# Kernel tuning notes

Hardware: AMD Instinct MI355X
Metric: run time of the kernel (lower is better)

The kernel has to match this reference:

```python
import jax, jax.numpy as jnp
import numpy as np

HIDDEN = 4096
NUM_HEADS = 32
HEAD_DIM = HIDDEN // NUM_HEADS  # 128


def apply_rope(x, cos, sin):
    # x: (B, H, S, D); cos/sin: (S, D//2)
    d2 = x.shape[-1] // 2
    x1, x2 = x[..., :d2], x[..., d2:]
    c = cos[None, None, :x.shape[2], :]
    s = sin[None, None, :x.shape[2], :]
    return jnp.concatenate([x1 * c - x2 * s, x2 * c + x1 * s], axis=-1)


def setup_inputs() -> dict:
    key = jax.random.key(0)
    ks = jax.random.split(key, 7)
    B, S = 2, 2048
    scale = 1.0 / np.sqrt(HIDDEN)
    return {
        "x": jax.random.normal(ks[0], (B, S, HIDDEN), dtype=jnp.float32),
        "cos": jax.random.normal(ks[1], (S, HEAD_DIM // 2), dtype=jnp.float32),
        "sin": jax.random.normal(ks[2], (S, HEAD_DIM // 2), dtype=jnp.float32),
        "wq": jax.random.normal(ks[3], (HIDDEN, HIDDEN), dtype=jnp.float32) * scale,
        "wk": jax.random.normal(ks[4], (HIDDEN, HIDDEN), dtype=jnp.float32) * scale,
        "wv": jax.random.normal(ks[5], (HIDDEN, HIDDEN), dtype=jnp.float32) * scale,
        "wo": jax.random.normal(ks[6], (HIDDEN, HIDDEN), dtype=jnp.float32) * scale,
    }


def reference(x, cos, sin, wq, wk, wv, wo):
    B, S, _ = x.shape
    # nn.Linear(x) = x @ W.T  (weights stored (out, in))
    def proj(w):
        t = jnp.einsum('bsd,ed->bse', x, w)
        return t.reshape(B, S, NUM_HEADS, HEAD_DIM).transpose(0, 2, 1, 3)
    q, k, v = proj(wq), proj(wk), proj(wv)
    q = apply_rope(q, cos, sin)
    k = apply_rope(k, cos, sin)
    scale = HEAD_DIM ** (-0.5)
    attn = jnp.einsum('bhqd,bhkd->bhqk', q, k) * scale  # (B,H,S,S)
    causal = jnp.tril(jnp.ones((S, S), dtype=bool))
    attn = jnp.where(causal[None, None], attn, -jnp.inf)
    attn = jax.nn.softmax(attn, axis=-1)
    out = jnp.einsum('bhqk,bhkd->bhqd', attn, v)
    out = out.transpose(0, 2, 1, 3).reshape(B, S, HIDDEN)
    return jnp.einsum('bsd,ed->bse', out, wo)
```

## Files before the change

### kernel.cpp

```cpp
#include <hip/hip_runtime.h>
#include <stdint.h>

#define DEV __device__ __forceinline__

typedef __attribute__((ext_vector_type(8))) short short8v;
typedef __attribute__((ext_vector_type(4))) short short4v;
typedef __attribute__((ext_vector_type(4))) float f32x4;
typedef __attribute__((ext_vector_type(16))) float f32x16;

DEV uint16_t f2bf(float f) {
  union { float f; uint32_t u; } x; x.f = f;
  return (uint16_t)((x.u + 0x7FFFu + ((x.u >> 16) & 1u)) >> 16);
}
DEV float bf2f(uint16_t v) {
  union { uint32_t u; float f; } x; x.u = ((uint32_t)v) << 16;
  return x.f;
}

DEV void gload_lds16(const uint16_t* g, uint16_t* l) {
  __builtin_amdgcn_global_load_lds(
      (const __attribute__((address_space(1))) uint32_t*)g,
      (__attribute__((address_space(3))) uint32_t*)l, 16, 0, 0);
}

__global__ void convert5_kernel(const float* __restrict__ x,
                                const float* __restrict__ wq,
                                const float* __restrict__ wk,
                                const float* __restrict__ wv,
                                const float* __restrict__ wo,
                                uint16_t* __restrict__ xb, uint16_t* __restrict__ wqb,
                                uint16_t* __restrict__ wkb, uint16_t* __restrict__ wvb,
                                uint16_t* __restrict__ wob, int n4) {
  const int which = blockIdx.y;
  const float* in = which == 0 ? x : which == 1 ? wq : which == 2 ? wk
                                   : which == 3 ? wv : wo;
  uint16_t* out = which == 0 ? xb : which == 1 ? wqb : which == 2 ? wkb
                                  : which == 3 ? wvb : wob;
  int i = blockIdx.x * blockDim.x + threadIdx.x;
  if (i >= n4) return;
  float4 v = reinterpret_cast<const float4*>(in)[i];
  short4v o;
  o[0] = (short)f2bf(v.x); o[1] = (short)f2bf(v.y);
  o[2] = (short)f2bf(v.z); o[3] = (short)f2bf(v.w);
  *reinterpret_cast<short4v*>(out + (size_t)i * 4) = o;
}

template <int F32OUT>
__global__ __launch_bounds__(512, 2) void gemm256_kernel(
    const uint16_t* __restrict__ A, const uint16_t* __restrict__ Bt,
    float* __restrict__ Cf, uint16_t* __restrict__ Cb, int M, int N, int K) {
  __shared__ uint16_t smem[65536];
  uint16_t* As0 = smem;
  uint16_t* As1 = smem + 16384;
  uint16_t* Bs0 = smem + 32768;
  uint16_t* Bs1 = smem + 49152;

  const int tid = threadIdx.x;
  const int lane = tid & 63, w = tid >> 6;
  const int ln16 = lane & 15, g = lane >> 4;
  const int wr = w >> 2, wc = w & 3;

  const int nbx = gridDim.x;
  int bid = blockIdx.y * nbx + blockIdx.x;
  int nb = nbx * gridDim.y;
  int cpx = nb >> 3;
  int sw = (bid & 7) * cpx + (bid >> 3);
  const int m0 = (sw / nbx) * 256, n0 = (sw % nbx) * 256;

  const int trow = tid >> 3;
  const int tcol = ((tid & 7) ^ (trow & 7)) * 8;
  const uint16_t* srcA = A + (size_t)(m0 + trow) * K + tcol;
  const int brow = (w >> 2) * 64 + (w & 3) * 8 + (lane >> 3);
  const int bcol = ((lane & 7) ^ ((lane >> 3) & 7)) * 8;
  const uint16_t* srcB = Bt + (size_t)(n0 + brow) * K + bcol;
  const int dstAw = w * 512;
  const int dstBw = ((w >> 2) * 64 + (w & 3) * 8) * 64;

#define STA(buf, q, kt) \
  gload_lds16(srcA + (size_t)((q) * 64) * K + (kt) * 64, (buf) + (q) * 4096 + dstAw)
#define STB(buf, nq, c, kt) \
  gload_lds16(srcB + (size_t)((c) * 128 + (nq) * 32) * K + (kt) * 64, \
              (buf) + ((c) * 128 + (nq) * 32) * 64 + dstBw)
#define LDA(buf, mq, mi, ks) \
  (*reinterpret_cast<const short8v*>( \
      (buf) + (wr * 128 + (mq) * 64 + (mi) * 16 + ln16) * 64 + \
      ((((ks) * 4 + g) ^ (ln16 & 7)) * 8)))
#define LDB(buf, nq, ni, ks) \
  (*reinterpret_cast<const short8v*>( \
      (buf) + (wc * 64 + (nq) * 32 + (ni) * 16 + ln16) * 64 + \
      ((((ks) * 4 + g) ^ (ln16 & 7)) * 8)))

  f32x4 acc[8][4];
#pragma unroll
  for (int i = 0; i < 8; ++i)
#pragma unroll
    for (int j = 0; j < 4; ++j) acc[i][j] = f32x4{0.f, 0.f, 0.f, 0.f};

  STA(As0, 0, 0); STA(As0, 2, 0); STA(As0, 1, 0); STA(As0, 3, 0);
  STB(Bs0, 0, 0, 0); STB(Bs0, 0, 1, 0); STB(Bs0, 1, 0, 0); STB(Bs0, 1, 1, 0);
  STA(As1, 0, 1); STA(As1, 2, 1);
  STB(Bs1, 0, 0, 1); STB(Bs1, 0, 1, 1); STB(Bs1, 1, 0, 1); STB(Bs1, 1, 1, 1);
  asm volatile("s_waitcnt vmcnt(6)" ::: "memory");
  __builtin_amdgcn_sched_barrier(0);
  __builtin_amdgcn_s_barrier();

  uint16_t *Ac = As0, *An = As1, *Bc = Bs0, *Bn = Bs1;
  short8v af[4][2], bf0[2][2], bf1[2][2];

  const int NT = K >> 6;
  for (int t = 0; t < NT; ++t) {
    const int k1 = (t + 1 < NT) ? t + 1 : NT - 1;
    const int k2 = (t + 2 < NT) ? t + 2 : NT - 1;
#pragma unroll
    for (int mi = 0; mi < 4; ++mi) { af[mi][0] = LDA(Ac, 0, mi, 0); af[mi][1] = LDA(Ac, 0, mi, 1); }
#pragma unroll
    for (int ni = 0; ni < 2; ++ni) { bf0[ni][0] = LDB(Bc, 0, ni, 0); bf0[ni][1] = LDB(Bc, 0, ni, 1); }
    STA(An, 1, k1); STA(An, 3, k1);
    __builtin_amdgcn_s_barrier();
    asm volatile("s_waitcnt lgkmcnt(0)" ::: "memory");
    __builtin_amdgcn_sched_barrier(0);
    __builtin_amdgcn_s_setprio(1);
#pragma unroll
    for (int ks = 0; ks < 2; ++ks)
#pragma unroll
      for (int mi = 0; mi < 4; ++mi)
#pragma unroll
        for (int ni = 0; ni < 2; ++ni)
          acc[mi][ni] = __builtin_amdgcn_mfma_f32_16x16x32_bf16(af[mi][ks], bf0[ni][ks], acc[mi][ni], 0, 0, 0);
    __builtin_amdgcn_s_setprio(0);
    __builtin_amdgcn_s_barrier();
#pragma unroll
    for (int ni = 0; ni < 2; ++ni) { bf1[ni][0] = LDB(Bc, 1, ni, 0); bf1[ni][1] = LDB(Bc, 1, ni, 1); }
    STA(Ac, 0, k2); STA(Ac, 2, k2);
    __builtin_amdgcn_s_barrier();
    asm volatile("s_waitcnt lgkmcnt(0)" ::: "memory");
    __builtin_amdgcn_sched_barrier(0);
    __builtin_amdgcn_s_setprio(1);
#pragma unroll
    for (int ks = 0; ks < 2; ++ks)
#pragma unroll
      for (int mi = 0; mi < 4; ++mi)
#pragma unroll
        for (int ni = 0; ni < 2; ++ni)
          acc[mi][2 + ni] = __builtin_amdgcn_mfma_f32_16x16x32_bf16(af[mi][ks], bf1[ni][ks], acc[mi][2 + ni], 0, 0, 0);
    __builtin_amdgcn_s_setprio(0);
    __builtin_amdgcn_s_barrier();
#pragma unroll
    for (int mi = 0; mi < 4; ++mi) { af[mi][0] = LDA(Ac, 1, mi, 0); af[mi][1] = LDA(Ac, 1, mi, 1); }
    STB(Bc, 0, 0, k2); STB(Bc, 0, 1, k2);
    __builtin_amdgcn_s_barrier();
    asm volatile("s_waitcnt lgkmcnt(0)" ::: "memory");
    __builtin_amdgcn_sched_barrier(0);
    __builtin_amdgcn_s_setprio(1);
#pragma unroll
    for (int ks = 0; ks < 2; ++ks)
#pragma unroll
      for (int mi = 0; mi < 4; ++mi)
#pragma unroll
        for (int ni = 0; ni < 2; ++ni)
          acc[4 + mi][2 + ni] = __builtin_amdgcn_mfma_f32_16x16x32_bf16(af[mi][ks], bf1[ni][ks], acc[4 + mi][2 + ni], 0, 0, 0);
    __builtin_amdgcn_s_setprio(0);
    __builtin_amdgcn_s_barrier();
    STB(Bc, 1, 0, k2); STB(Bc, 1, 1, k2);
    __builtin_amdgcn_s_barrier();
    __builtin_amdgcn_s_setprio(1);
#pragma unroll
    for (int ks = 0; ks < 2; ++ks)
#pragma unroll
      for (int mi = 0; mi < 4; ++mi)
#pragma unroll
        for (int ni = 0; ni < 2; ++ni)
          acc[4 + mi][ni] = __builtin_amdgcn_mfma_f32_16x16x32_bf16(af[mi][ks], bf0[ni][ks], acc[4 + mi][ni], 0, 0, 0);
    __builtin_amdgcn_s_setprio(0);
    asm volatile("s_waitcnt vmcnt(6)" ::: "memory");
    __builtin_amdgcn_sched_barrier(0);
    __builtin_amdgcn_s_barrier();
    uint16_t* tp = Ac; Ac = An; An = tp;
    tp = Bc; Bc = Bn; Bn = tp;
  }

#pragma unroll
  for (int gmi = 0; gmi < 8; ++gmi)
#pragma unroll
    for (int r = 0; r < 4; ++r) {
      int row = m0 + wr * 128 + gmi * 16 + g * 4 + r;
#pragma unroll
      for (int gni = 0; gni < 4; ++gni) {
        int col = n0 + wc * 64 + gni * 16 + ln16;
        if (F32OUT)
          Cf[(size_t)row * N + col] = acc[gmi][gni][r];
        else
          Cb[(size_t)row * N + col] = (uint16_t)f2bf(acc[gmi][gni][r]);
      }
    }
#undef STA
#undef STB
#undef LDA
#undef LDB
}

__global__ void rope_kernel(uint16_t* __restrict__ buf,
                            const float* __restrict__ cost,
                            const float* __restrict__ sint) {
  int idx = blockIdx.x * blockDim.x + threadIdx.x;
  int j8 = idx & 7;
  int h = (idx >> 3) & 31;
  int s = (idx >> 8) & 2047;
  int b = idx >> 19;
  size_t base = ((size_t)(b * 2048 + s)) * 4096 + h * 128 + j8 * 8;
  short8v x1 = *reinterpret_cast<const short8v*>(buf + base);
  short8v x2 = *reinterpret_cast<const short8v*>(buf + base + 64);
  float4 c0 = *reinterpret_cast<const float4*>(cost + s * 64 + j8 * 8);
  float4 c1 = *reinterpret_cast<const float4*>(cost + s * 64 + j8 * 8 + 4);
  float4 s0 = *reinterpret_cast<const float4*>(sint + s * 64 + j8 * 8);
  float4 s1 = *reinterpret_cast<const float4*>(sint + s * 64 + j8 * 8 + 4);
  float c[8] = {c0.x, c0.y, c0.z, c0.w, c1.x, c1.y, c1.z, c1.w};
  float sn[8] = {s0.x, s0.y, s0.z, s0.w, s1.x, s1.y, s1.z, s1.w};
  short8v o1, o2;
#pragma unroll
  for (int e = 0; e < 8; ++e) {
    float a = bf2f((uint16_t)x1[e]);
    float bb = bf2f((uint16_t)x2[e]);
    o1[e] = (short)f2bf(a * c[e] - bb * sn[e]);
    o2[e] = (short)f2bf(bb * c[e] + a * sn[e]);
  }
  *reinterpret_cast<short8v*>(buf + base) = o1;
  *reinterpret_cast<short8v*>(buf + base + 64) = o2;
}

__global__ __launch_bounds__(256, 2) void flash_kernel(
    const uint16_t* __restrict__ Q, const uint16_t* __restrict__ K,
    const uint16_t* __restrict__ V, uint16_t* __restrict__ O) {
  constexpr int S = 2048, HID = 4096;
  __shared__ uint16_t Ks[64 * 128];
  __shared__ uint16_t Vt[128 * 64];

  const int tid = threadIdx.x;
  const int lane = tid & 63, w = tid >> 6;
  const int l31 = lane & 31, hi = lane >> 5;
  const int bh = blockIdx.y;
  const int b = bh >> 5, h = bh & 31;
  const int bt = 15 - blockIdx.x;
  const int q0 = bt * 128;
  const int q0w = q0 + w * 32;
  const size_t base = (size_t)b * S * HID + (size_t)h * 128;
  const int swz = (l31 & 7) << 3;

  short8v qf[8];
  {
    const uint16_t* qrow = Q + base + (size_t)(q0w + l31) * HID + hi * 8;
#pragma unroll
    for (int c = 0; c < 8; ++c)
      qf[c] = *reinterpret_cast<const short8v*>(qrow + c * 16);
  }

  f32x16 o[4];
#pragma unroll
  for (int db = 0; db < 4; ++db)
#pragma unroll
    for (int r = 0; r < 16; ++r) o[db][r] = 0.f;
  float m_run = -1e30f, l_run = 0.f;
  const float cl2e = 0.12751025f;

  const int ntiles = bt * 2 + 2;
  for (int kt = 0; kt < ntiles; ++kt) {
    const int kb = kt * 64;
    if (kt > 0) __syncthreads();
#pragma unroll
    for (int i = 0; i < 4; ++i) {
      int row = i * 16 + (tid >> 4);
      int colc = (tid & 15) * 8;
      short8v kv = *reinterpret_cast<const short8v*>(
          K + base + (size_t)(kb + row) * HID + colc);
      *reinterpret_cast<short8v*>(Ks + row * 128 + (colc ^ ((row & 7) << 3))) = kv;
    }
    {
      int k4 = tid & 15, dc = tid >> 4;
      short8v v0 = *reinterpret_cast<const short8v*>(V + base + (size_t)(kb + 4 * k4 + 0) * HID + dc * 8);
      short8v v1 = *reinterpret_cast<const short8v*>(V + base + (size_t)(kb + 4 * k4 + 1) * HID + dc * 8);
      short8v v2 = *reinterpret_cast<const short8v*>(V + base + (size_t)(kb + 4 * k4 + 2) * HID + dc * 8);
      short8v v3 = *reinterpret_cast<const short8v*>(V + base + (size_t)(kb + 4 * k4 + 3) * HID + dc * 8);
#pragma unroll
      for (int e = 0; e < 8; ++e) {
        int row = dc * 8 + e;
        short4v pk; pk[0] = v0[e]; pk[1] = v1[e]; pk[2] = v2[e]; pk[3] = v3[e];
        *reinterpret_cast<short4v*>(Vt + row * 64 + ((k4 * 4) ^ ((row & 7) << 3))) = pk;
      }
    }
    __syncthreads();

    if (kb <= q0w + 31) {
      f32x16 s0, s1;
#pragma unroll
      for (int r = 0; r < 16; ++r) { s0[r] = 0.f; s1[r] = 0.f; }
#pragma unroll
      for (int c = 0; c < 8; ++c) {
        int col = c * 16 + hi * 8;
        short8v kf0 = *reinterpret_cast<const short8v*>(Ks + l31 * 128 + (col ^ swz));
        short8v kf1 = *reinterpret_cast<const short8v*>(Ks + (32 + l31) * 128 + (col ^ swz));
        s0 = __builtin_amdgcn_mfma_f32_32x32x16_bf16(kf0, qf[c], s0, 0, 0, 0);
        s1 = __builtin_amdgcn_mfma_f32_32x32x16_bf16(kf1, qf[c], s1, 0, 0, 0);
      }
#pragma unroll
      for (int r = 0; r < 16; ++r) { s0[r] *= cl2e; s1[r] *= cl2e; }
      if (kb + 63 > q0w) {
        const int qg = q0w + l31;
#pragma unroll
        for (int r = 0; r < 16; ++r) {
          int kl = (r & 3) + 8 * (r >> 2) + 4 * hi;
          if (kb + kl > qg) s0[r] = -1e30f;
          if (kb + 32 + kl > qg) s1[r] = -1e30f;
        }
      }
      float mx = s0[0];
#pragma unroll
      for (int r = 1; r < 16; ++r) mx = fmaxf(mx, s0[r]);
#pragma unroll
      for (int r = 0; r < 16; ++r) mx = fmaxf(mx, s1[r]);
      mx = fmaxf(mx, __shfl_xor(mx, 32));
      if (__any(mx > m_run + 8.0f)) {
        float nm = fmaxf(m_run, mx);
        float f = __builtin_amdgcn_exp2f(m_run - nm);
        l_run *= f;
#pragma unroll
        for (int db = 0; db < 4; ++db)
#pragma unroll
          for (int r = 0; r < 16; ++r) o[db][r] *= f;
        m_run = nm;
      }
      float rs = 0.f;
#pragma unroll
      for (int r = 0; r < 16; ++r) { s0[r] = __builtin_amdgcn_exp2f(s0[r] - m_run); rs += s0[r]; }
#pragma unroll
      for (int r = 0; r < 16; ++r) { s1[r] = __builtin_amdgcn_exp2f(s1[r] - m_run); rs += s1[r]; }
      rs += __shfl_xor(rs, 32);
      l_run += rs;
      uint32_t c0[8], c1[8];
#pragma unroll
      for (int i = 0; i < 4; ++i) {
        asm("v_cvt_pk_bf16_f32 %0, %1, %2" : "=v"(c0[i])     : "v"(s0[4 * i]),     "v"(s0[4 * i + 1]));
        asm("v_cvt_pk_bf16_f32 %0, %1, %2" : "=v"(c1[i])     : "v"(s0[4 * i + 2]), "v"(s0[4 * i + 3]));
        asm("v_cvt_pk_bf16_f32 %0, %1, %2" : "=v"(c0[4 + i]) : "v"(s1[4 * i]),     "v"(s1[4 * i + 1]));
        asm("v_cvt_pk_bf16_f32 %0, %1, %2" : "=v"(c1[4 + i]) : "v"(s1[4 * i + 2]), "v"(s1[4 * i + 3]));
      }
      short8v pa[4];
#pragma unroll
      for (int t = 0; t < 4; ++t) {
        int st = t >> 1, ts = t & 1;
        uint32_t a0 = c0[st * 4 + 2 * ts],     a1 = c1[st * 4 + 2 * ts];
        uint32_t b0 = c0[st * 4 + 2 * ts + 1], b1 = c1[st * 4 + 2 * ts + 1];
        uint32_t sb0 = (uint32_t)__shfl_xor((int)b0, 32);
        uint32_t sb1 = (uint32_t)__shfl_xor((int)b1, 32);
        uint32_t sa0 = (uint32_t)__shfl_xor((int)a0, 32);
        uint32_t sa1 = (uint32_t)__shfl_xor((int)a1, 32);
        union { uint32_t u[4]; short8v v; } pk;
        pk.u[0] = hi ? sb0 : a0;
        pk.u[1] = hi ? sb1 : a1;
        pk.u[2] = hi ? b0 : sa0;
        pk.u[3] = hi ? b1 : sa1;
        pa[t] = pk.v;
      }
#pragma unroll
      for (int t = 0; t < 4; ++t) {
        int col = t * 16 + hi * 8;
#pragma unroll
        for (int db = 0; db < 4; ++db) {
          short8v vf = *reinterpret_cast<const short8v*>(
              Vt + (db * 32 + l31) * 64 + (col ^ swz));
          o[db] = __builtin_amdgcn_mfma_f32_32x32x16_bf16(vf, pa[t], o[db], 0, 0, 0);
        }
      }
    }
  }

  float inv = 1.f / l_run;
  uint16_t* orow = O + base + (size_t)(q0w + l31) * HID;
#pragma unroll
  for (int db = 0; db < 4; ++db)
#pragma unroll
    for (int rq = 0; rq < 4; ++rq) {
      short4v st4;
#pragma unroll
      for (int e = 0; e < 4; ++e) st4[e] = (short)f2bf(o[db][rq * 4 + e] * inv);
      *reinterpret_cast<short4v*>(orow + db * 32 + rq * 8 + hi * 4) = st4;
    }
}

extern "C" void kernel_launch(void* const* d_in, const int* in_sizes, int n_in,
                              void* d_out, int out_size, void* d_ws, size_t ws_size,
                              hipStream_t stream) {
  const float* x    = (const float*)d_in[0];
  const float* cosb = (const float*)d_in[1];
  const float* sinb = (const float*)d_in[2];
  const float* wq   = (const float*)d_in[3];
  const float* wk   = (const float*)d_in[4];
  const float* wv   = (const float*)d_in[5];
  const float* wo   = (const float*)d_in[6];
  float* out = (float*)d_out;

  const size_t BUF = 33554432;
  if (ws_size < 8 * BUF) return;
  char* ws = (char*)d_ws;
  uint16_t* xb  = (uint16_t*)(ws + 0 * BUF);
  uint16_t* wqb = (uint16_t*)(ws + 1 * BUF);
  uint16_t* wkb = (uint16_t*)(ws + 2 * BUF);
  uint16_t* wvb = (uint16_t*)(ws + 3 * BUF);
  uint16_t* wob = (uint16_t*)(ws + 4 * BUF);
  uint16_t* qb  = (uint16_t*)(ws + 5 * BUF);
  uint16_t* kb  = (uint16_t*)(ws + 6 * BUF);
  uint16_t* vb  = (uint16_t*)(ws + 7 * BUF);
  uint16_t* ab  = xb;

  const int nElem = 2 * 2048 * 4096;
  dim3 cgrid(nElem / 4 / 256, 5);
  convert5_kernel<<<cgrid, 256, 0, stream>>>(x, wq, wk, wv, wo,
                                             xb, wqb, wkb, wvb, wob, nElem / 4);

  dim3 ggrid(16, 16), gblk(512);
  gemm256_kernel<0><<<ggrid, gblk, 0, stream>>>(xb, wqb, nullptr, qb, 4096, 4096, 4096);
  gemm256_kernel<0><<<ggrid, gblk, 0, stream>>>(xb, wkb, nullptr, kb, 4096, 4096, 4096);
  gemm256_kernel<0><<<ggrid, gblk, 0, stream>>>(xb, wvb, nullptr, vb, 4096, 4096, 4096);

  dim3 rgrid(1048576 / 256);
  rope_kernel<<<rgrid, 256, 0, stream>>>(qb, cosb, sinb);
  rope_kernel<<<rgrid, 256, 0, stream>>>(kb, cosb, sinb);

  dim3 fgrid(16, 64);
  flash_kernel<<<fgrid, 256, 0, stream>>>(qb, kb, vb, ab);

  gemm256_kernel<1><<<ggrid, gblk, 0, stream>>>(ab, wob, out, nullptr, 4096, 4096, 4096);
}
```

Baseline: 786.9 us.

## Prefetch next K/V tile into registers during compute and raise MFMA priority

The flash attention loop now issues global loads for the next K/V tile into registers before computing on the current tile, then writes them to LDS after a barrier. This hides global memory latency behind the QK and PV MFMA work instead of stalling at the start of each iteration. It also wraps the MFMA blocks in s_setprio to favour matrix issue across waves. The cost is higher register pressure from the prefetch buffers, which could hurt occupancy under launch_bounds(256,2).

```diff
diff --git a/kernel.cpp b/kernel.cpp
--- a/kernel.cpp
+++ b/kernel.cpp
@@ -246,6 +246,11 @@
   const size_t base = (size_t)b * S * HID + (size_t)h * 128;
   const int swz = (l31 & 7) << 3;
 
+  const int ksr = tid >> 4;
+  const int ksc = (tid & 15) * 8;
+  const int vk4 = tid & 15;
+  const int vdc = tid >> 4;
+
   short8v qf[8];
   {
     const uint16_t* qrow = Q + base + (size_t)(q0w + l31) * HID + hi * 8;
@@ -262,37 +267,50 @@
   float m_run = -1e30f, l_run = 0.f;
   const float cl2e = 0.12751025f;
 
+  short8v kp[4], vp[4];
+
+#pragma unroll
+  for (int i = 0; i < 4; ++i)
+    kp[i] = *reinterpret_cast<const short8v*>(
+        K + base + (size_t)(i * 16 + ksr) * HID + ksc);
+#pragma unroll
+  for (int j = 0; j < 4; ++j)
+    vp[j] = *reinterpret_cast<const short8v*>(
+        V + base + (size_t)(4 * vk4 + j) * HID + vdc * 8);
+#pragma unroll
+  for (int i = 0; i < 4; ++i) {
+    int row = i * 16 + ksr;
+    *reinterpret_cast<short8v*>(Ks + row * 128 + (ksc ^ ((row & 7) << 3))) = kp[i];
+  }
+#pragma unroll
+  for (int e = 0; e < 8; ++e) {
+    int row = vdc * 8 + e;
+    short4v pk; pk[0] = vp[0][e]; pk[1] = vp[1][e]; pk[2] = vp[2][e]; pk[3] = vp[3][e];
+    *reinterpret_cast<short4v*>(Vt + row * 64 + ((vk4 * 4) ^ ((row & 7) << 3))) = pk;
+  }
+  __syncthreads();
+
   const int ntiles = bt * 2 + 2;
   for (int kt = 0; kt < ntiles; ++kt) {
     const int kb = kt * 64;
-    if (kt > 0) __syncthreads();
-#pragma unroll
-    for (int i = 0; i < 4; ++i) {
-      int row = i * 16 + (tid >> 4);
-      int colc = (tid & 15) * 8;
-      short8v kv = *reinterpret_cast<const short8v*>(
-          K + base + (size_t)(kb + row) * HID + colc);
-      *reinterpret_cast<short8v*>(Ks + row * 128 + (colc ^ ((row & 7) << 3))) = kv;
+    const bool havenext = (kt + 1 < ntiles);
+    if (havenext) {
+      const int kb2 = kb + 64;
+#pragma unroll
+      for (int i = 0; i < 4; ++i)
+        kp[i] = *reinterpret_cast<const short8v*>(
+            K + base + (size_t)(kb2 + i * 16 + ksr) * HID + ksc);
+#pragma unroll
+      for (int j = 0; j < 4; ++j)
+        vp[j] = *reinterpret_cast<const short8v*>(
+            V + base + (size_t)(kb2 + 4 * vk4 + j) * HID + vdc * 8);
     }
-    {
-      int k4 = tid & 15, dc = tid >> 4;
-      short8v v0 = *reinterpret_cast<const short8v*>(V + base + (size_t)(kb + 4 * k4 + 0) * HID + dc * 8);
-      short8v v1 = *reinterpret_cast<const short8v*>(V + base + (size_t)(kb + 4 * k4 + 1) * HID + dc * 8);
-      short8v v2 = *reinterpret_cast<const short8v*>(V + base + (size_t)(kb + 4 * k4 + 2) * HID + dc * 8);
-      short8v v3 = *reinterpret_cast<const short8v*>(V + base + (size_t)(kb + 4 * k4 + 3) * HID + dc * 8);
-#pragma unroll
-      for (int e = 0; e < 8; ++e) {
-        int row = dc * 8 + e;
-        short4v pk; pk[0] = v0[e]; pk[1] = v1[e]; pk[2] = v2[e]; pk[3] = v3[e];
-        *reinterpret_cast<short4v*>(Vt + row * 64 + ((k4 * 4) ^ ((row & 7) << 3))) = pk;
-      }
-    }
-    __syncthreads();
 
     if (kb <= q0w + 31) {
       f32x16 s0, s1;
 #pragma unroll
       for (int r = 0; r < 16; ++r) { s0[r] = 0.f; s1[r] = 0.f; }
+      __builtin_amdgcn_s_setprio(1);
 #pragma unroll
       for (int c = 0; c < 8; ++c) {
         int col = c * 16 + hi * 8;
@@ -301,6 +319,7 @@
         s0 = __builtin_amdgcn_mfma_f32_32x32x16_bf16(kf0, qf[c], s0, 0, 0, 0);
         s1 = __builtin_amdgcn_mfma_f32_32x32x16_bf16(kf1, qf[c], s1, 0, 0, 0);
       }
+      __builtin_amdgcn_s_setprio(0);
 #pragma unroll
       for (int r = 0; r < 16; ++r) { s0[r] *= cl2e; s1[r] *= cl2e; }
       if (kb + 63 > q0w) {
@@ -360,6 +379,7 @@
         pk.u[3] = hi ? b1 : sa1;
         pa[t] = pk.v;
       }
+      __builtin_amdgcn_s_setprio(1);
 #pragma unroll
       for (int t = 0; t < 4; ++t) {
         int col = t * 16 + hi * 8;
@@ -370,6 +390,22 @@
           o[db] = __builtin_amdgcn_mfma_f32_32x32x16_bf16(vf, pa[t], o[db], 0, 0, 0);
         }
       }
+      __builtin_amdgcn_s_setprio(0);
+    }
+    __syncthreads();
+    if (havenext) {
+#pragma unroll
+      for (int i = 0; i < 4; ++i) {
+        int row = i * 16 + ksr;
+        *reinterpret_cast<short8v*>(Ks + row * 128 + (ksc ^ ((row & 7) << 3))) = kp[i];
+      }
+#pragma unroll
+      for (int e = 0; e < 8; ++e) {
+        int row = vdc * 8 + e;
+        short4v pk; pk[0] = vp[0][e]; pk[1] = vp[1][e]; pk[2] = vp[2][e]; pk[3] = vp[3][e];
+        *reinterpret_cast<short4v*>(Vt + row * 64 + ((vk4 * 4) ^ ((row & 7) << 3))) = pk;
+      }
+      __syncthreads();
     }
   }
 
```

Result: faster. 713.8 us (-9.3%).
